# Optimization experiments

Measured on AMD Instinct MI355X. Metric: run time of the kernel, lower is better.

Reference implementation:

```python
import jax, jax.numpy as jnp
import numpy as np


def setup_inputs() -> dict:
    key = jax.random.key(0)
    k1, k2 = jax.random.split(key)
    x1 = jax.random.normal(k1, (256, 128, 32, 32), dtype=jnp.float32)   # queries [B,C,h,w]
    x2 = jax.random.normal(k2, (16, 8, 128, 32, 32), dtype=jnp.float32)  # supports [n_way,shot,C,h,w]
    return {"x1": x1, "x2": x2}


def reference(x1, x2):
    # --- cal_covariance: per-class channel covariance over all support pixels ---
    W, S, C, h, w = x2.shape
    sup = x2.transpose(0, 2, 1, 3, 4).reshape(W, C, S * h * w)  # [W, C, S*h*w]
    sup = sup - sup.mean(axis=2, keepdims=True)
    cova = jnp.einsum('wci,wdi->wcd', sup, sup) / (S * h * w - 1)  # [W, C, C]

    # --- cal_similarity: diagonal of q^T Cova q with per-channel L2-normalized query ---
    B, C, h, w = x1.shape
    q = x1.reshape(B, C, h * w)
    q = q / jnp.linalg.norm(q, axis=2, keepdims=True)  # norm over spatial dim per channel
    # diag_i = q[:, i]^T Cova q[:, i]; compute diagonal directly (no (hw)x(hw) matrix)
    sim = jnp.einsum('bci,wcd,bdi->bwi', q, cova, q)  # [B, W, h*w]
    return sim.reshape(B, W * h * w)
```

## Files before the change

### kernel.cpp

```cpp
#include <hip/hip_runtime.h>

typedef _Float16 half8 __attribute__((ext_vector_type(8)));
typedef _Float16 half4 __attribute__((ext_vector_type(4)));
typedef float    f32x4 __attribute__((ext_vector_type(4)));

#define W_CLS 16
#define SHOT  8
#define C_CH  128
#define HW    1024
#define NSAMP (SHOT*HW)
#define B_Q   256

__device__ __forceinline__ void gload_lds16(const _Float16* g, _Float16* l) {
    __builtin_amdgcn_global_load_lds((const __attribute__((address_space(1))) unsigned int*)g,
                                     (__attribute__((address_space(3))) unsigned int*)l,
                                     16, 0, 0);
}


__global__ __launch_bounds__(512) void covarn_kernel(const float* __restrict__ x2,
                                                     const float* __restrict__ x1,
                                                     float* __restrict__ PG,
                                                     float* __restrict__ pmean,
                                                     float* __restrict__ rn) {
    __shared__ _Float16 XT[2][128*72];
    __shared__ float mred[128][4];
    int tid = threadIdx.x;

    if (blockIdx.x >= 256) {
        int rid  = blockIdx.x - 256;
        int row  = rid * 8 + (tid >> 6);
        int lane = tid & 63;
        const f32x4* pr = (const f32x4*)(x1 + (size_t)row * HW);
        float s = 0.f;
        #pragma unroll
        for (int it = 0; it < 4; ++it) {
            f32x4 v = pr[lane + it * 64];
            s += v[0]*v[0] + v[1]*v[1] + v[2]*v[2] + v[3]*v[3];
        }
        #pragma unroll
        for (int off = 32; off; off >>= 1) s += __shfl_xor(s, off, 64);
        if (lane == 0) rn[row] = 1.0f / sqrtf(s);
        return;
    }

    int w = blockIdx.x >> 4, ks = blockIdx.x & 15;
    int s = ks >> 1, p00 = (ks & 1) * 512;
    int c = tid >> 2, ph = (tid & 3) * 16;
    const float* src = x2 + (((size_t)(w*SHOT + s))*C_CH + c)*HW + p00 + ph;
    int lane = tid & 63, wv = tid >> 6;
    int lr = lane & 15, lg = lane >> 4;
    int mt0 = (wv & 3)*2, nt0 = (wv >> 2)*4;

    float msum = 0.f;
    f32x4 acc[2][4];
    #pragma unroll
    for (int mm = 0; mm < 2; ++mm)
        #pragma unroll
        for (int nn = 0; nn < 4; ++nn) acc[mm][nn] = (f32x4){0.f,0.f,0.f,0.f};

    float4 rg[4];
    #pragma unroll
    for (int j = 0; j < 4; ++j) rg[j] = *(const float4*)(src + j*4);
    #pragma unroll
    for (int j = 0; j < 4; ++j) {
        msum += rg[j].x + rg[j].y + rg[j].z + rg[j].w;
        half4 h = {(_Float16)rg[j].x, (_Float16)rg[j].y, (_Float16)rg[j].z, (_Float16)rg[j].w};
        *(half4*)(&XT[0][c*72 + ph + j*4]) = h;
    }
    __syncthreads();

    for (int ch = 0; ch < 8; ++ch) {
        int buf = ch & 1;
        if (ch < 7) {
            #pragma unroll
            for (int j = 0; j < 4; ++j) rg[j] = *(const float4*)(src + (ch+1)*64 + j*4);
        }
        const _Float16* xb = XT[buf];
        #pragma unroll
        for (int kk = 0; kk < 2; ++kk) {
            half8 Bv[4], Av[2];
            #pragma unroll
            for (int nn = 0; nn < 4; ++nn)
                Bv[nn] = *(const half8*)(xb + ((nt0+nn)*16 + lr)*72 + kk*32 + lg*8);
            #pragma unroll
            for (int mm = 0; mm < 2; ++mm)
                Av[mm] = *(const half8*)(xb + ((mt0+mm)*16 + lr)*72 + kk*32 + lg*8);
            #pragma unroll
            for (int mm = 0; mm < 2; ++mm)
                #pragma unroll
                for (int nn = 0; nn < 4; ++nn)
                    acc[mm][nn] = __builtin_amdgcn_mfma_f32_16x16x32_f16(Av[mm], Bv[nn], acc[mm][nn], 0,0,0);
        }
        if (ch < 7) {
            #pragma unroll
            for (int j = 0; j < 4; ++j) {
                msum += rg[j].x + rg[j].y + rg[j].z + rg[j].w;
                half4 h = {(_Float16)rg[j].x, (_Float16)rg[j].y, (_Float16)rg[j].z, (_Float16)rg[j].w};
                *(half4*)(&XT[buf^1][c*72 + ph + j*4]) = h;
            }
        }
        __syncthreads();
    }

    mred[c][tid & 3] = msum;
    __syncthreads();
    if (tid < 128)
        pmean[((size_t)w*16 + ks)*128 + tid] = mred[tid][0]+mred[tid][1]+mred[tid][2]+mred[tid][3];

    float* pg = PG + ((size_t)w*16 + ks)*16384;
    #pragma unroll
    for (int mm = 0; mm < 2; ++mm)
        #pragma unroll
        for (int nn = 0; nn < 4; ++nn)
            #pragma unroll
            for (int r = 0; r < 4; ++r) {
                int cr = (mt0+mm)*16 + lg*4 + r;
                int d  = (nt0+nn)*16 + lr;
                pg[cr*128 + d] = acc[mm][nn][r];
            }
}

__global__ __launch_bounds__(256) void cova_reduce(const float* __restrict__ PG,
                                                   const float* __restrict__ pmean,
                                                   _Float16* __restrict__ Uh) {
    __shared__ float ms[128];
    int t = threadIdx.x;
    int w = blockIdx.x >> 3, rg = blockIdx.x & 7;
    if (t < 128) {
        float sum = 0.f;
        for (int ks = 0; ks < 16; ++ks) sum += pmean[((size_t)w*16 + ks)*128 + t];
        ms[t] = sum * (1.0f/NSAMP);
    }
    __syncthreads();
    const float* pg = PG + (size_t)w*16*16384;
    #pragma unroll
    for (int it = 0; it < 8; ++it) {
        int e = it*256 + t;
        int r = rg*16 + (e >> 7), d = e & 127;
        float g = 0.f;
        for (int ks = 0; ks < 16; ++ks) g += pg[(size_t)ks*16384 + r*128 + d];
        float val = (g - (float)NSAMP*ms[r]*ms[d]) * (1.0f/(NSAMP-1));
        float uval = (d > r) ? val : ((d == r) ? 0.5f*val : 0.0f);
        Uh[((size_t)w*128 + r)*128 + d] = (_Float16)uval;
    }
}

__global__ __launch_bounds__(512) void qconv4_kernel(const float* __restrict__ x1,
                                                     const float* __restrict__ rn,
                                                     _Float16* __restrict__ qf) {
    __shared__ _Float16 T[128*258];
    int tid = threadIdx.x, lane = tid & 63, wv = tid >> 6;
    int b = blockIdx.x >> 2, ic = blockIdx.x & 3;
    const float* xb = x1 + (size_t)b * C_CH * HW + ic*256;
    const float* rnb = rn + b * C_CH;

    #pragma unroll
    for (int cc = 0; cc < 16; ++cc) {
        int c = wv*16 + cc;
        float sc = rnb[c];
        f32x4 v = *(const f32x4*)(xb + (size_t)c * HW + lane*4);
        half4 h = {(_Float16)(v[0]*sc), (_Float16)(v[1]*sc),
                   (_Float16)(v[2]*sc), (_Float16)(v[3]*sc)};
        *(half4*)(&T[c*258 + lane*4]) = h;
    }
    __syncthreads();

    #pragma unroll
    for (int it = 0; it < 8; ++it) {
        int slot = it*512 + tid;
        int tl = slot >> 8;
        int kk = (slot >> 6) & 3;
        int ln = slot & 63;
        int i_loc = tl*16 + (ln & 15);
        int c0 = kk*32 + (ln >> 4)*8;
        half8 pk;
        #pragma unroll
        for (int e = 0; e < 8; ++e) pk[e] = T[(c0+e)*258 + i_loc];
        *(half8*)(qf + (((size_t)b*64 + ic*16 + tl)*4 + kk)*512 + ln*8) = pk;
    }
}

#define TR 4
__global__ __launch_bounds__(256, 3) void sim_kernel(const _Float16* __restrict__ qf,
                                                     const _Float16* __restrict__ Uh,
                                                     float* __restrict__ out) {
    __shared__ _Float16 stage[2][TR*2048];
    int tid = threadIdx.x, lane = tid & 63, wv = tid >> 6;
    int lr = lane & 15, lg = lane >> 4;
    int b = blockIdx.x & 255, wg = blockIdx.x >> 8;
    int w = wg*4 + wv;

    half8 A[20];
    {
        const _Float16* Ub = Uh + (size_t)w*C_CH*C_CH + (size_t)lr*C_CH + lg*8;
        int idx = 0;
        #pragma unroll
        for (int kk = 0; kk < 4; ++kk)
            #pragma unroll
            for (int m = 0; m <= 2*kk+1; ++m) {
                A[idx] = *(const half8*)(Ub + (size_t)m*16*C_CH + kk*32);
                ++idx;
            }
    }

    const _Float16* qfb = qf + (size_t)b * 131072;

    #pragma unroll
    for (int k = 0; k < 4; ++k)
        gload_lds16(qfb + tid*8 + k*2048, &stage[0][tid*8 + k*2048]);
    __syncthreads();

    int offD0 = (lg>>1)*128 + lr*8 + (lg&1)*4;
    float* ob = out + ((size_t)b*W_CLS + w)*HW;
    int cur = 0;

    for (int r = 0; r < 16; ++r) {
        if (r < 15) {
            const _Float16* gsrc = qfb + (size_t)(r+1)*(TR*2048);
            #pragma unroll
            for (int k = 0; k < 4; ++k)
                gload_lds16(gsrc + tid*8 + k*2048, &stage[cur^1][tid*8 + k*2048]);
        }
        #pragma unroll
        for (int ti = 0; ti < TR; ++ti) {
            const _Float16* tb = &stage[cur][ti*2048];
            half8 B[4];
            #pragma unroll
            for (int kk = 0; kk < 4; ++kk)
                B[kk] = *(const half8*)(tb + kk*512 + lane*8);
            half4 D[8];
            #pragma unroll
            for (int m = 0; m < 8; ++m)
                D[m] = *(const half4*)(tb + (m>>1)*512 + (m&1)*256 + offD0);
            f32x4 acc[8];
            #pragma unroll
            for (int m = 0; m < 8; ++m) acc[m] = (f32x4){0.f,0.f,0.f,0.f};
            __builtin_amdgcn_s_setprio(1);
            {
                int idx = 0;
                #pragma unroll
                for (int kk = 0; kk < 4; ++kk)
                    #pragma unroll
                    for (int m = 0; m <= 2*kk+1; ++m) {
                        acc[m] = __builtin_amdgcn_mfma_f32_16x16x32_f16(A[idx], B[kk], acc[m], 0, 0, 0);
                        ++idx;
                    }
            }
            __builtin_amdgcn_s_setprio(0);
            float s = 0.f;
            #pragma unroll
            for (int m = 0; m < 8; ++m) {
                s = fmaf((float)D[m][0], acc[m][0], s);
                s = fmaf((float)D[m][1], acc[m][1], s);
                s = fmaf((float)D[m][2], acc[m][2], s);
                s = fmaf((float)D[m][3], acc[m][3], s);
            }
            s += __shfl_xor(s, 16, 64);
            s += __shfl_xor(s, 32, 64);
            if (lane < 16) ob[(r*TR + ti)*16 + lr] = 2.0f * s;
        }
        __syncthreads();
        cur ^= 1;
    }
}
#undef TR


__global__ __launch_bounds__(256) void rnorm_kernel(const float* __restrict__ x1,
                                                    float* __restrict__ rn) {
    int row  = blockIdx.x * 4 + (threadIdx.x >> 6);
    int lane = threadIdx.x & 63;
    const float4* p = (const float4*)(x1 + (size_t)row * HW);
    float s = 0.f;
    #pragma unroll
    for (int it = 0; it < 4; ++it) {
        float4 v = p[lane + it * 64];
        s += v.x*v.x + v.y*v.y + v.z*v.z + v.w*v.w;
    }
    for (int off = 32; off; off >>= 1) s += __shfl_down(s, off, 64);
    if (lane == 0) rn[row] = 1.0f / sqrtf(s);
}

__global__ __launch_bounds__(256) void mean_kernel_f(const float* __restrict__ x2,
                                                     float* __restrict__ mean) {
    int wc = blockIdx.x;
    int w  = wc >> 7, c = wc & 127;
    const float* base = x2 + ((size_t)(w * SHOT) * C_CH + c) * HW;
    int tid = threadIdx.x;
    float sum = 0.f;
    for (int s = 0; s < SHOT; ++s) {
        const float* row = base + (size_t)s * C_CH * HW;
        for (int p = tid; p < HW; p += 256) sum += row[p];
    }
    for (int off = 32; off; off >>= 1) sum += __shfl_down(sum, off, 64);
    __shared__ float red[4];
    int lane = tid & 63, wv = tid >> 6;
    if (lane == 0) red[wv] = sum;
    __syncthreads();
    if (tid == 0) mean[wc] = (red[0] + red[1] + red[2] + red[3]) * (1.0f / NSAMP);
}

__global__ __launch_bounds__(256) void cova_kernel_f(const float* __restrict__ x2,
                                                     const float* __restrict__ mean,
                                                     _Float16* __restrict__ covah) {
    int bid = blockIdx.x;
    int w  = bid >> 4;
    int c0 = ((bid >> 2) & 3) * 32;
    int d0 = (bid & 3) * 32;
    __shared__ float As[32][33];
    __shared__ float Bs[32][33];
    int tid = threadIdx.x;
    int ty = tid >> 4, tx = tid & 15;
    int lrr = tid >> 3, lc = (tid & 7) * 4;
    const float* base = x2 + (size_t)w * SHOT * C_CH * HW;
    float acc00 = 0.f, acc01 = 0.f, acc10 = 0.f, acc11 = 0.f;
    for (int k0 = 0; k0 < NSAMP; k0 += 32) {
        int s = k0 >> 10, p = k0 & 1023;
        const float4 a4 = *(const float4*)(base + ((size_t)s * C_CH + (c0 + lrr)) * HW + p + lc);
        const float4 b4 = *(const float4*)(base + ((size_t)s * C_CH + (d0 + lrr)) * HW + p + lc);
        As[lrr][lc+0] = a4.x; As[lrr][lc+1] = a4.y; As[lrr][lc+2] = a4.z; As[lrr][lc+3] = a4.w;
        Bs[lrr][lc+0] = b4.x; Bs[lrr][lc+1] = b4.y; Bs[lrr][lc+2] = b4.z; Bs[lrr][lc+3] = b4.w;
        __syncthreads();
        #pragma unroll
        for (int kk = 0; kk < 32; ++kk) {
            float a0 = As[ty*2][kk],   a1 = As[ty*2+1][kk];
            float b0 = Bs[tx*2][kk],   b1 = Bs[tx*2+1][kk];
            acc00 = fmaf(a0, b0, acc00);
            acc01 = fmaf(a0, b1, acc01);
            acc10 = fmaf(a1, b0, acc10);
            acc11 = fmaf(a1, b1, acc11);
        }
        __syncthreads();
    }
    const float inv = 1.0f / (NSAMP - 1);
    int c = c0 + ty * 2, d = d0 + tx * 2;
    float mc0 = mean[w*128 + c],     mc1 = mean[w*128 + c + 1];
    float md0 = mean[w*128 + d],     md1 = mean[w*128 + d + 1];
    _Float16* o = covah + ((size_t)w * 128 + c) * 128 + d;
    o[0]   = (_Float16)((acc00 - (float)NSAMP * mc0 * md0) * inv);
    o[1]   = (_Float16)((acc01 - (float)NSAMP * mc0 * md1) * inv);
    o[128] = (_Float16)((acc10 - (float)NSAMP * mc1 * md0) * inv);
    o[129] = (_Float16)((acc11 - (float)NSAMP * mc1 * md1) * inv);
}

#define LDQ 136
__global__ __launch_bounds__(512) void sim_kernel_f(const float* __restrict__ x1,
                                                    const _Float16* __restrict__ Ch,
                                                    const float* __restrict__ rn,
                                                    float* __restrict__ out) {
    __shared__ _Float16 qT[128][LDQ];
    __shared__ float simbuf[2][128];
    int tid = threadIdx.x;
    int bq  = blockIdx.x;
    int b   = bq >> 3;
    int i0  = (bq & 7) * 128;
    {
        int c  = tid >> 2;
        int iq = (tid & 3) * 32;
        const float* src = x1 + ((size_t)b * C_CH + c) * HW + i0 + iq;
        float scale = rn[b * C_CH + c];
        #pragma unroll
        for (int j4 = 0; j4 < 8; ++j4) {
            f32x4 v = *(const f32x4*)(src + j4 * 4);
            qT[iq + j4*4 + 0][c] = (_Float16)(v[0] * scale);
            qT[iq + j4*4 + 1][c] = (_Float16)(v[1] * scale);
            qT[iq + j4*4 + 2][c] = (_Float16)(v[2] * scale);
            qT[iq + j4*4 + 3][c] = (_Float16)(v[3] * scale);
        }
    }
    __syncthreads();
    int lane = tid & 63;
    int wv   = tid >> 6;
    int mh   = wv >> 2;
    int nq   = wv & 3;
    int d0w  = mh * 64;
    int iw   = nq * 32;
    int lr   = lane & 15;
    int lg   = lane >> 4;
    float qd[4][2][4];
    #pragma unroll
    for (int m = 0; m < 4; ++m)
        #pragma unroll
        for (int n = 0; n < 2; ++n) {
            half4 hq = *(const half4*)&qT[iw + n*16 + lr][d0w + m*16 + lg*4];
            qd[m][n][0] = (float)hq[0];
            qd[m][n][1] = (float)hq[1];
            qd[m][n][2] = (float)hq[2];
            qd[m][n][3] = (float)hq[3];
        }
    for (int w = 0; w < W_CLS; ++w) {
        const _Float16* Cw = Ch + (size_t)w * C_CH * C_CH;
        half8 A[4][4];
        #pragma unroll
        for (int m = 0; m < 4; ++m)
            #pragma unroll
            for (int k = 0; k < 4; ++k)
                A[m][k] = *(const half8*)(Cw + (size_t)(d0w + m*16 + lr) * C_CH + k*32 + lg*8);
        f32x4 acc[4][2];
        #pragma unroll
        for (int m = 0; m < 4; ++m)
            #pragma unroll
            for (int n = 0; n < 2; ++n)
                acc[m][n] = (f32x4){0.f, 0.f, 0.f, 0.f};
        #pragma unroll
        for (int k = 0; k < 4; ++k) {
            #pragma unroll
            for (int n = 0; n < 2; ++n) {
                half8 Bf = *(const half8*)&qT[iw + n*16 + lr][k*32 + lg*8];
                #pragma unroll
                for (int m = 0; m < 4; ++m)
                    acc[m][n] = __builtin_amdgcn_mfma_f32_16x16x32_f16(A[m][k], Bf, acc[m][n], 0, 0, 0);
            }
        }
        float s0 = 0.f, s1 = 0.f;
        #pragma unroll
        for (int m = 0; m < 4; ++m) {
            #pragma unroll
            for (int r = 0; r < 4; ++r) {
                s0 = fmaf(qd[m][0][r], acc[m][0][r], s0);
                s1 = fmaf(qd[m][1][r], acc[m][1][r], s1);
            }
        }
        s0 += __shfl_xor(s0, 16); s0 += __shfl_xor(s0, 32);
        s1 += __shfl_xor(s1, 16); s1 += __shfl_xor(s1, 32);
        if (lane < 16) {
            simbuf[mh][iw + 0*16 + lane] = s0;
            simbuf[mh][iw + 1*16 + lane] = s1;
        }
        __syncthreads();
        if (tid < 128)
            out[((size_t)b * W_CLS + w) * HW + i0 + tid] = simbuf[0][tid] + simbuf[1][tid];
        __syncthreads();
    }
}


extern "C" void kernel_launch(void* const* d_in, const int* in_sizes, int n_in,
                              void* d_out, int out_size, void* d_ws, size_t ws_size,
                              hipStream_t stream) {
    (void)in_sizes; (void)n_in; (void)out_size;
    const float* x1 = (const float*)d_in[0];
    const float* x2 = (const float*)d_in[1];
    float* out = (float*)d_out;

    char* ws = (char*)d_ws;
    const size_t OFF_QF  = 0;
    const size_t OFF_PG  = 67108864;
    const size_t OFF_PM  = OFF_PG  + 16777216;
    const size_t OFF_UH  = OFF_PM  + 131072;
    const size_t OFF_RN  = OFF_UH  + 524288;
    const size_t NEED    = OFF_RN  + 131072;

    if (ws_size >= NEED) {
        _Float16* qf  = (_Float16*)(ws + OFF_QF);
        float*    PG  = (float*)(ws + OFF_PG);
        float*    pm  = (float*)(ws + OFF_PM);
        _Float16* Uh  = (_Float16*)(ws + OFF_UH);
        float*    rn  = (float*)(ws + OFF_RN);
        covarn_kernel<<<4352, 512, 0, stream>>>(x2, x1, PG, pm, rn);
        cova_reduce  <<<128,  256, 0, stream>>>(PG, pm, Uh);
        qconv4_kernel<<<1024, 512, 0, stream>>>(x1, rn, qf);
        sim_kernel   <<<1024, 256, 0, stream>>>(qf, Uh, out);
    } else {
        float*    mean = (float*)ws;
        float*    rn   = mean + W_CLS*C_CH;
        _Float16* Ch   = (_Float16*)(rn + B_Q*C_CH);
        mean_kernel_f<<<W_CLS*C_CH,  256, 0, stream>>>(x2, mean);
        cova_kernel_f<<<W_CLS*16,    256, 0, stream>>>(x2, mean, Ch);
        rnorm_kernel <<<B_Q*C_CH/4,  256, 0, stream>>>(x1, rn);
        sim_kernel_f <<<B_Q*8,       512, 0, stream>>>(x1, Ch, rn, out);
    }
}
```

Measured before the change: 192.6 us.

## Fuse query norm into qconv, merge covariance reduce, read D from global

The per-channel inverse norm of x1 moves out of the covariance kernel and into the query-conversion kernel, which now handles one batch per block and keeps the norms in LDS. The covariance reduction runs as extra blocks of that same launch, so there are three launches instead of four. In sim_kernel the D operands are now loaded straight from global (L2) rather than from the LDS stage. This removes a launch and the rn round trip through memory, but cuts qconv parallelism from 1024 blocks to 256 and reads x1 twice per block.

```diff
diff --git a/kernel.cpp b/kernel.cpp
--- a/kernel.cpp
+++ b/kernel.cpp
@@ -18,31 +18,12 @@
 }
 
 
-__global__ __launch_bounds__(512) void covarn_kernel(const float* __restrict__ x2,
-                                                     const float* __restrict__ x1,
-                                                     float* __restrict__ PG,
-                                                     float* __restrict__ pmean,
-                                                     float* __restrict__ rn) {
+__global__ __launch_bounds__(512) void cova_kernel(const float* __restrict__ x2,
+                                                   float* __restrict__ PG,
+                                                   float* __restrict__ pmean) {
     __shared__ _Float16 XT[2][128*72];
     __shared__ float mred[128][4];
     int tid = threadIdx.x;
-
-    if (blockIdx.x >= 256) {
-        int rid  = blockIdx.x - 256;
-        int row  = rid * 8 + (tid >> 6);
-        int lane = tid & 63;
-        const f32x4* pr = (const f32x4*)(x1 + (size_t)row * HW);
-        float s = 0.f;
-        #pragma unroll
-        for (int it = 0; it < 4; ++it) {
-            f32x4 v = pr[lane + it * 64];
-            s += v[0]*v[0] + v[1]*v[1] + v[2]*v[2] + v[3]*v[3];
-        }
-        #pragma unroll
-        for (int off = 32; off; off >>= 1) s += __shfl_xor(s, off, 64);
-        if (lane == 0) rn[row] = 1.0f / sqrtf(s);
-        return;
-    }
 
     int w = blockIdx.x >> 4, ks = blockIdx.x & 15;
     int s = ks >> 1, p00 = (ks & 1) * 512;
@@ -121,63 +102,83 @@
             }
 }
 
-__global__ __launch_bounds__(256) void cova_reduce(const float* __restrict__ PG,
-                                                   const float* __restrict__ pmean,
-                                                   _Float16* __restrict__ Uh) {
-    __shared__ float ms[128];
-    int t = threadIdx.x;
-    int w = blockIdx.x >> 3, rg = blockIdx.x & 7;
-    if (t < 128) {
-        float sum = 0.f;
-        for (int ks = 0; ks < 16; ++ks) sum += pmean[((size_t)w*16 + ks)*128 + t];
-        ms[t] = sum * (1.0f/NSAMP);
-    }
-    __syncthreads();
-    const float* pg = PG + (size_t)w*16*16384;
-    #pragma unroll
-    for (int it = 0; it < 8; ++it) {
-        int e = it*256 + t;
-        int r = rg*16 + (e >> 7), d = e & 127;
-        float g = 0.f;
-        for (int ks = 0; ks < 16; ++ks) g += pg[(size_t)ks*16384 + r*128 + d];
-        float val = (g - (float)NSAMP*ms[r]*ms[d]) * (1.0f/(NSAMP-1));
-        float uval = (d > r) ? val : ((d == r) ? 0.5f*val : 0.0f);
-        Uh[((size_t)w*128 + r)*128 + d] = (_Float16)uval;
-    }
-}
-
-__global__ __launch_bounds__(512) void qconv4_kernel(const float* __restrict__ x1,
-                                                     const float* __restrict__ rn,
-                                                     _Float16* __restrict__ qf) {
+__global__ __launch_bounds__(512) void qcr_kernel(const float* __restrict__ x1,
+                                                  _Float16* __restrict__ qf,
+                                                  const float* __restrict__ PG,
+                                                  const float* __restrict__ pmean,
+                                                  _Float16* __restrict__ Uh) {
+    if (blockIdx.x >= 256) {
+        __shared__ float ms[128];
+        int t = threadIdx.x;
+        int bid = blockIdx.x - 256;
+        int w = bid >> 3, rg = bid & 7;
+        if (t < 128) {
+            float sum = 0.f;
+            for (int ks = 0; ks < 16; ++ks) sum += pmean[((size_t)w*16 + ks)*128 + t];
+            ms[t] = sum * (1.0f/NSAMP);
+        }
+        __syncthreads();
+        const float* pg = PG + (size_t)w*16*16384;
+        #pragma unroll
+        for (int it = 0; it < 4; ++it) {
+            int e = it*512 + t;
+            int r = rg*16 + (e >> 7), d = e & 127;
+            float g = 0.f;
+            for (int ks = 0; ks < 16; ++ks) g += pg[(size_t)ks*16384 + r*128 + d];
+            float val = (g - (float)NSAMP*ms[r]*ms[d]) * (1.0f/(NSAMP-1));
+            float uval = (d > r) ? val : ((d == r) ? 0.5f*val : 0.0f);
+            Uh[((size_t)w*128 + r)*128 + d] = (_Float16)uval;
+        }
+        return;
+    }
+
     __shared__ _Float16 T[128*258];
+    __shared__ float rnL[128];
     int tid = threadIdx.x, lane = tid & 63, wv = tid >> 6;
-    int b = blockIdx.x >> 2, ic = blockIdx.x & 3;
-    const float* xb = x1 + (size_t)b * C_CH * HW + ic*256;
-    const float* rnb = rn + b * C_CH;
+    int b = blockIdx.x;
+    const float* xb = x1 + (size_t)b * C_CH * HW;
 
     #pragma unroll
     for (int cc = 0; cc < 16; ++cc) {
         int c = wv*16 + cc;
-        float sc = rnb[c];
-        f32x4 v = *(const f32x4*)(xb + (size_t)c * HW + lane*4);
-        half4 h = {(_Float16)(v[0]*sc), (_Float16)(v[1]*sc),
-                   (_Float16)(v[2]*sc), (_Float16)(v[3]*sc)};
-        *(half4*)(&T[c*258 + lane*4]) = h;
-    }
-    __syncthreads();
-
-    #pragma unroll
-    for (int it = 0; it < 8; ++it) {
-        int slot = it*512 + tid;
-        int tl = slot >> 8;
-        int kk = (slot >> 6) & 3;
-        int ln = slot & 63;
-        int i_loc = tl*16 + (ln & 15);
-        int c0 = kk*32 + (ln >> 4)*8;
-        half8 pk;
-        #pragma unroll
-        for (int e = 0; e < 8; ++e) pk[e] = T[(c0+e)*258 + i_loc];
-        *(half8*)(qf + (((size_t)b*64 + ic*16 + tl)*4 + kk)*512 + ln*8) = pk;
+        const f32x4* row = (const f32x4*)(xb + (size_t)c * HW);
+        float s = 0.f;
+        #pragma unroll
+        for (int j = 0; j < 4; ++j) {
+            f32x4 v = row[lane + j*64];
+            s += v[0]*v[0] + v[1]*v[1] + v[2]*v[2] + v[3]*v[3];
+        }
+        #pragma unroll
+        for (int off = 32; off; off >>= 1) s += __shfl_xor(s, off, 64);
+        if (lane == 0) rnL[c] = 1.0f / sqrtf(s);
+    }
+    __syncthreads();
+
+    for (int ic = 0; ic < 4; ++ic) {
+        #pragma unroll
+        for (int cc = 0; cc < 16; ++cc) {
+            int c = wv*16 + cc;
+            f32x4 v = *(const f32x4*)(xb + (size_t)c * HW + ic*256 + lane*4);
+            float sc = rnL[c];
+            half4 h = {(_Float16)(v[0]*sc), (_Float16)(v[1]*sc),
+                       (_Float16)(v[2]*sc), (_Float16)(v[3]*sc)};
+            *(half4*)(&T[c*258 + lane*4]) = h;
+        }
+        __syncthreads();
+        #pragma unroll
+        for (int it = 0; it < 8; ++it) {
+            int slot = it*512 + tid;
+            int tl = slot >> 8;
+            int kk = (slot >> 6) & 3;
+            int ln = slot & 63;
+            int i_loc = tl*16 + (ln & 15);
+            int c0 = kk*32 + (ln >> 4)*8;
+            half8 pk;
+            #pragma unroll
+            for (int e = 0; e < 8; ++e) pk[e] = T[(c0+e)*258 + i_loc];
+            *(half8*)(qf + (((size_t)b*64 + ic*16 + tl)*4 + kk)*512 + ln*8) = pk;
+        }
+        __syncthreads();
     }
 }
 
@@ -224,15 +225,16 @@
         }
         #pragma unroll
         for (int ti = 0; ti < TR; ++ti) {
+            const _Float16* gt = qfb + (size_t)(r*TR + ti)*2048;
+            half4 D[8];
+            #pragma unroll
+            for (int m = 0; m < 8; ++m)
+                D[m] = *(const half4*)(gt + (m>>1)*512 + (m&1)*256 + offD0);
             const _Float16* tb = &stage[cur][ti*2048];
             half8 B[4];
             #pragma unroll
             for (int kk = 0; kk < 4; ++kk)
                 B[kk] = *(const half8*)(tb + kk*512 + lane*8);
-            half4 D[8];
-            #pragma unroll
-            for (int m = 0; m < 8; ++m)
-                D[m] = *(const half4*)(tb + (m>>1)*512 + (m&1)*256 + offD0);
             f32x4 acc[8];
             #pragma unroll
             for (int m = 0; m < 8; ++m) acc[m] = (f32x4){0.f,0.f,0.f,0.f};
@@ -457,11 +459,9 @@
         float*    PG  = (float*)(ws + OFF_PG);
         float*    pm  = (float*)(ws + OFF_PM);
         _Float16* Uh  = (_Float16*)(ws + OFF_UH);
-        float*    rn  = (float*)(ws + OFF_RN);
-        covarn_kernel<<<4352, 512, 0, stream>>>(x2, x1, PG, pm, rn);
-        cova_reduce  <<<128,  256, 0, stream>>>(PG, pm, Uh);
-        qconv4_kernel<<<1024, 512, 0, stream>>>(x1, rn, qf);
-        sim_kernel   <<<1024, 256, 0, stream>>>(qf, Uh, out);
+        cova_kernel<<<256,  512, 0, stream>>>(x2, PG, pm);
+        qcr_kernel <<<384,  512, 0, stream>>>(x1, qf, PG, pm, Uh);
+        sim_kernel <<<1024, 256, 0, stream>>>(qf, Uh, out);
     } else {
         float*    mean = (float*)ws;
         float*    rn   = mean + W_CLS*C_CH;
```

Measured after the change: 175.2 us. -9.0%, faster.
